# Performance work log

Hardware: AMD Instinct MI355X
Metric: run time of the kernel (lower is better)

The kernel has to match this reference:

```python
import jax, jax.numpy as jnp
import numpy as np

B, N, H = 2, 160, 256
F = 512  # num_hidden_fc
C3 = 3 * H  # concatenated modality feature
C6 = 2 * C3  # pairwise feature


def setup_inputs() -> dict:
    key = jax.random.key(0)
    ks = jax.random.split(key, 16)
    s1 = 1.0 / np.sqrt(C6)
    s2 = 1.0 / np.sqrt(F)
    inp = {
        "geometry": jax.random.normal(ks[0], (B, N, H), jnp.float32),
        "appearance": jax.random.normal(ks[1], (B, N, H), jnp.float32),
        "content": jax.random.normal(ks[2], (B, N, H), jnp.float32),
    }
    for i, name in enumerate(["cell", "row", "col"]):
        inp[f"{name}_W1"] = jax.random.normal(ks[3 + 4 * i], (C6, F), jnp.float32) * s1
        inp[f"{name}_b1"] = jnp.zeros((F,), jnp.float32)
        inp[f"{name}_W2"] = jax.random.normal(ks[4 + 4 * i], (F, 2), jnp.float32) * s2
        inp[f"{name}_b2"] = jnp.zeros((2,), jnp.float32)
    return inp


def _head(x, W1, b1, W2, b2):
    h = jax.nn.relu(jnp.einsum("bpc,cf->bpf", x, W1) + b1)
    return jax.nn.softmax(jnp.einsum("bpf,fk->bpk", h, W2) + b2, axis=-1)


def reference(geometry, appearance, content,
              cell_W1, cell_b1, cell_W2, cell_b2,
              row_W1, row_b1, row_W2, row_b2,
              col_W1, col_b1, col_W2, col_b2):
    emb = jnp.concatenate([geometry, appearance, content], axis=-1)  # (B,N,3H)
    b, n, c = emb.shape
    # pairs[b,i,j] = concat(emb[b,j], emb[b,i])  (matches unsqueeze(1)/unsqueeze(2) order)
    e_j = jnp.broadcast_to(emb[:, None, :, :], (b, n, n, c))
    e_i = jnp.broadcast_to(emb[:, :, None, :], (b, n, n, c))
    emb_pairs = jnp.concatenate([e_j, e_i], axis=-1).reshape(b, n * n, 2 * c)
    cell_logits = _head(emb_pairs, cell_W1, cell_b1, cell_W2, cell_b2)
    row_logits = _head(emb_pairs, row_W1, row_b1, row_W2, row_b2)
    col_logits = _head(emb_pairs, col_W1, col_b1, col_W2, col_b2)
    return cell_logits, row_logits, col_logits, emb_pairs
```

## Files before the change

### kernel.cpp

```cpp
#include <hip/hip_runtime.h>

#define NB 2
#define NN 160
#define NPAIR (NN*NN)
#define OUT_PAIRS_OFF 307200

__global__ __launch_bounds__(256) void proj_fp32_kernel(
    const float* __restrict__ geo, const float* __restrict__ app,
    const float* __restrict__ con,
    const float* __restrict__ w1c, const float* __restrict__ w1r,
    const float* __restrict__ w1l,
    const float* __restrict__ b1c, const float* __restrict__ b1r,
    const float* __restrict__ b1l,
    float* __restrict__ proj)
{
    __shared__ float As[64][17];
    __shared__ float Bs[16][68];

    const int tid = threadIdx.x;
    const int m0 = blockIdx.x * 64;
    const int n0 = blockIdx.y * 64;
    const int t  = n0 >> 10;
    const int s  = (n0 >> 9) & 1;
    const int f0 = n0 & 511;

    const float* w1 = (t == 0) ? w1c : ((t == 1) ? w1r : w1l);
    const float* b1 = (t == 0) ? b1c : ((t == 1) ? b1r : b1l);

    const int ty = tid >> 4, tx = tid & 15;
    const int ar = tid >> 2, ac = (tid & 3) * 4;
    const int bk = tid >> 4, bn = (tid & 15) * 4;

    float acc[4][4] = {};

    for (int k0 = 0; k0 < 768; k0 += 16) {
        {
            const int c = k0 + ac;
            const int m = c >> 8, off = c & 255;
            const float* src = ((m == 0) ? geo : (m == 1) ? app : con)
                               + (size_t)(m0 + ar) * 256 + off;
            const float4 v = *(const float4*)src;
            As[ar][ac + 0] = v.x; As[ar][ac + 1] = v.y;
            As[ar][ac + 2] = v.z; As[ar][ac + 3] = v.w;
        }
        {
            const float4 v = *(const float4*)(
                w1 + (size_t)(s * 768 + k0 + bk) * 512 + f0 + bn);
            Bs[bk][bn + 0] = v.x; Bs[bk][bn + 1] = v.y;
            Bs[bk][bn + 2] = v.z; Bs[bk][bn + 3] = v.w;
        }
        __syncthreads();

        #pragma unroll
        for (int k = 0; k < 16; ++k) {
            const float4 b = *(const float4*)&Bs[k][tx * 4];
            const float a0 = As[ty * 4 + 0][k];
            const float a1 = As[ty * 4 + 1][k];
            const float a2 = As[ty * 4 + 2][k];
            const float a3 = As[ty * 4 + 3][k];
            acc[0][0] += a0 * b.x; acc[0][1] += a0 * b.y;
            acc[0][2] += a0 * b.z; acc[0][3] += a0 * b.w;
            acc[1][0] += a1 * b.x; acc[1][1] += a1 * b.y;
            acc[1][2] += a1 * b.z; acc[1][3] += a1 * b.w;
            acc[2][0] += a2 * b.x; acc[2][1] += a2 * b.y;
            acc[2][2] += a2 * b.z; acc[2][3] += a2 * b.w;
            acc[3][0] += a3 * b.x; acc[3][1] += a3 * b.y;
            acc[3][2] += a3 * b.z; acc[3][3] += a3 * b.w;
        }
        __syncthreads();
    }

    float4 bias = {0.f, 0.f, 0.f, 0.f};
    if (s == 0) bias = *(const float4*)&b1[f0 + tx * 4];

    #pragma unroll
    for (int r = 0; r < 4; ++r) {
        float4 o;
        o.x = acc[r][0] + bias.x; o.y = acc[r][1] + bias.y;
        o.z = acc[r][2] + bias.z; o.w = acc[r][3] + bias.w;
        *(float4*)&proj[(size_t)((t * 2 + s) * 320 + m0 + ty * 4 + r) * 512
                        + f0 + tx * 4] = o;
    }
}

__global__ __launch_bounds__(64) void heads_kernel(
    const float* __restrict__ proj,
    const float* __restrict__ w2c, const float* __restrict__ b2c,
    const float* __restrict__ w2r, const float* __restrict__ b2r,
    const float* __restrict__ w2l, const float* __restrict__ b2l,
    float* __restrict__ out)
{
    __shared__ float P1s[8][516];
    __shared__ float P2s[8][516];
    __shared__ float w2s[1024];
    __shared__ float b2s[2];

    const int tid = threadIdx.x;
    const int bid = blockIdx.x;
    const int b   = bid / 400;
    const int rem = bid - b * 400;
    const int it  = rem / 20;
    const int jt  = rem - it * 20;
    const int i0 = it * 8, j0 = jt * 8;
    const int ii = tid >> 3, jj = tid & 7;

    #pragma unroll
    for (int t = 0; t < 3; ++t) {
        const float* w2 = (t == 0) ? w2c : ((t == 1) ? w2r : w2l);
        const float* b2 = (t == 0) ? b2c : ((t == 1) ? b2r : b2l);

        for (int u = tid; u < 2048; u += 64) {
            const int tile = u >> 10;
            const int r    = (u >> 7) & 7;
            const int f4   = u & 127;
            const int p    = b * 160 + (tile ? (i0 + r) : (j0 + r));
            const float4 v = *(const float4*)(
                proj + ((size_t)((t * 2 + tile) * 320 + p)) * 512 + f4 * 4);
            float* dst = tile ? &P2s[r][f4 * 4] : &P1s[r][f4 * 4];
            *(float4*)dst = v;
        }
        for (int u = tid; u < 256; u += 64)
            *(float4*)&w2s[u * 4] = *(const float4*)(w2 + u * 4);
        if (tid < 2) b2s[tid] = b2[tid];
        __syncthreads();

        float a0 = b2s[0], a1 = b2s[1];
        for (int f = 0; f < 512; f += 4) {
            const float4 p1 = *(const float4*)&P1s[jj][f];
            const float4 p2 = *(const float4*)&P2s[ii][f];
            const float4 wA = *(const float4*)&w2s[f * 2];
            const float4 wB = *(const float4*)&w2s[f * 2 + 4];
            const float h0 = fmaxf(p1.x + p2.x, 0.f);
            const float h1 = fmaxf(p1.y + p2.y, 0.f);
            const float h2 = fmaxf(p1.z + p2.z, 0.f);
            const float h3 = fmaxf(p1.w + p2.w, 0.f);
            a0 += h0 * wA.x + h1 * wA.z + h2 * wB.x + h3 * wB.z;
            a1 += h0 * wA.y + h1 * wA.w + h2 * wB.y + h3 * wB.w;
        }

        const float mx = fmaxf(a0, a1);
        const float e0 = __expf(a0 - mx);
        const float e1 = __expf(a1 - mx);
        const float rs = 1.f / (e0 + e1);

        const int pr = b * 25600 + (i0 + ii) * 160 + (j0 + jj);
        float2 o; o.x = e0 * rs; o.y = e1 * rs;
        ((float2*)out)[t * 51200 + pr] = o;
        __syncthreads();
    }
}

__global__ __launch_bounds__(256) void pairs_kernel(
    const float* __restrict__ geo, const float* __restrict__ app,
    const float* __restrict__ con,
    float4* __restrict__ outp)
{
    const int idx = blockIdx.x * 256 + threadIdx.x;
    const int row = idx / 384;
    const int c   = idx - row * 384;
    const int b   = row / 25600;
    const int rem = row - b * 25600;
    const int i   = rem / 160;
    const int j   = rem - i * 160;

    int cc = c, pt = j;
    if (c >= 192) { pt = i; cc = c - 192; }
    const int m   = cc >> 6;
    const int off = cc & 63;
    const float* src = ((m == 0) ? geo : (m == 1) ? app : con)
                       + ((size_t)(b * 160 + pt)) * 256 + off * 4;

    outp[idx] = *(const float4*)src;
}

extern "C" void kernel_launch(void* const* d_in, const int* in_sizes, int n_in,
                              void* d_out, int out_size, void* d_ws, size_t ws_size,
                              hipStream_t stream)
{
    const float* geo = (const float*)d_in[0];
    const float* app = (const float*)d_in[1];
    const float* con = (const float*)d_in[2];
    const float* w1c = (const float*)d_in[3];
    const float* b1c = (const float*)d_in[4];
    const float* w2c = (const float*)d_in[5];
    const float* b2c = (const float*)d_in[6];
    const float* w1r = (const float*)d_in[7];
    const float* b1r = (const float*)d_in[8];
    const float* w2r = (const float*)d_in[9];
    const float* b2r = (const float*)d_in[10];
    const float* w1l = (const float*)d_in[11];
    const float* b1l = (const float*)d_in[12];
    const float* w2l = (const float*)d_in[13];
    const float* b2l = (const float*)d_in[14];

    float* out = (float*)d_out;

    float* proj = out + OUT_PAIRS_OFF;

    proj_fp32_kernel<<<dim3(5, 48), 256, 0, stream>>>(
        geo, app, con, w1c, w1r, w1l, b1c, b1r, b1l, proj);

    heads_kernel<<<800, 64, 0, stream>>>(
        proj, w2c, b2c, w2r, b2r, w2l, b2l, out);

    pairs_kernel<<<76800, 256, 0, stream>>>(
        geo, app, con, (float4*)(out + OUT_PAIRS_OFF));
}
```

Before: 446.0 us.

## Use bf16 MFMA for projection, fuse pair writes into heads, sigmoid-difference softmax

The fp32 tiled projection GEMM is replaced with a one-wave bf16 MFMA kernel (16x16x32) that converts inputs and weights to bf16 in registers. The pair-broadcast output copy is merged into the heads kernel, so each of the 800 blocks writes its own 64 rows of emb_pairs, and proj moves to workspace memory. The 2-way softmax now reduces to a single logit difference, with one dot product and a sigmoid. Together these remove one launch and roughly halve the head arithmetic, at the cost of bf16 rounding in the projection and much less parallelism for the 157 MB pair write, which now uses only 800 blocks of 64 threads.

```diff
diff --git a/kernel.cpp b/kernel.cpp
--- a/kernel.cpp
+++ b/kernel.cpp
@@ -5,7 +5,17 @@
 #define NPAIR (NN*NN)
 #define OUT_PAIRS_OFF 307200
 
-__global__ __launch_bounds__(256) void proj_fp32_kernel(
+typedef __attribute__((ext_vector_type(8))) short bf16x8;
+typedef __attribute__((ext_vector_type(4))) float f32x4;
+
+static __device__ __forceinline__ ushort f2bf(float x) {
+    union { float f; uint u; } c; c.f = x;
+    uint u = c.u;
+    u += 0x7fffu + ((u >> 16) & 1u);
+    return (ushort)(u >> 16);
+}
+
+__global__ __launch_bounds__(64) void proj_mfma_kernel(
     const float* __restrict__ geo, const float* __restrict__ app,
     const float* __restrict__ con,
     const float* __restrict__ w1c, const float* __restrict__ w1r,
@@ -14,76 +24,69 @@
     const float* __restrict__ b1l,
     float* __restrict__ proj)
 {
-    __shared__ float As[64][17];
-    __shared__ float Bs[16][68];
-
-    const int tid = threadIdx.x;
-    const int m0 = blockIdx.x * 64;
-    const int n0 = blockIdx.y * 64;
-    const int t  = n0 >> 10;
-    const int s  = (n0 >> 9) & 1;
+    const int lane = threadIdx.x;
+    const int m0 = blockIdx.x * 32;
+    const int n0 = blockIdx.y * 16;
+    const int t = n0 >> 10;
+    const int s = (n0 >> 9) & 1;
     const int f0 = n0 & 511;
 
     const float* w1 = (t == 0) ? w1c : ((t == 1) ? w1r : w1l);
     const float* b1 = (t == 0) ? b1c : ((t == 1) ? b1r : b1l);
 
-    const int ty = tid >> 4, tx = tid & 15;
-    const int ar = tid >> 2, ac = (tid & 3) * 4;
-    const int bk = tid >> 4, bn = (tid & 15) * 4;
+    const int col = lane & 15;
+    const int quad = lane >> 4;
 
-    float acc[4][4] = {};
+    f32x4 acc0 = {0.f, 0.f, 0.f, 0.f};
+    f32x4 acc1 = {0.f, 0.f, 0.f, 0.f};
 
-    for (int k0 = 0; k0 < 768; k0 += 16) {
-        {
-            const int c = k0 + ac;
-            const int m = c >> 8, off = c & 255;
-            const float* src = ((m == 0) ? geo : (m == 1) ? app : con)
-                               + (size_t)(m0 + ar) * 256 + off;
-            const float4 v = *(const float4*)src;
-            As[ar][ac + 0] = v.x; As[ar][ac + 1] = v.y;
-            As[ar][ac + 2] = v.z; As[ar][ac + 3] = v.w;
-        }
-        {
-            const float4 v = *(const float4*)(
-                w1 + (size_t)(s * 768 + k0 + bk) * 512 + f0 + bn);
-            Bs[bk][bn + 0] = v.x; Bs[bk][bn + 1] = v.y;
-            Bs[bk][bn + 2] = v.z; Bs[bk][bn + 3] = v.w;
-        }
-        __syncthreads();
+    const float* wbase = w1 + (size_t)(s * 768) * 512 + f0 + col;
+    const int p0 = m0 + col;
+    const int p1 = p0 + 16;
 
+    for (int k0 = 0; k0 < 768; k0 += 32) {
+        const int klane = k0 + quad * 8;
+        const int mod = klane >> 8;
+        const int off = klane & 255;
+        const float* src = (mod == 0) ? geo : ((mod == 1) ? app : con);
+
+        const float4 a0lo = *(const float4*)(src + (size_t)p0 * 256 + off);
+        const float4 a0hi = *(const float4*)(src + (size_t)p0 * 256 + off + 4);
+        const float4 a1lo = *(const float4*)(src + (size_t)p1 * 256 + off);
+        const float4 a1hi = *(const float4*)(src + (size_t)p1 * 256 + off + 4);
+
+        bf16x8 af0, af1, bfrag;
+        af0[0] = (short)f2bf(a0lo.x); af0[1] = (short)f2bf(a0lo.y);
+        af0[2] = (short)f2bf(a0lo.z); af0[3] = (short)f2bf(a0lo.w);
+        af0[4] = (short)f2bf(a0hi.x); af0[5] = (short)f2bf(a0hi.y);
+        af0[6] = (short)f2bf(a0hi.z); af0[7] = (short)f2bf(a0hi.w);
+        af1[0] = (short)f2bf(a1lo.x); af1[1] = (short)f2bf(a1lo.y);
+        af1[2] = (short)f2bf(a1lo.z); af1[3] = (short)f2bf(a1lo.w);
+        af1[4] = (short)f2bf(a1hi.x); af1[5] = (short)f2bf(a1hi.y);
+        af1[6] = (short)f2bf(a1hi.z); af1[7] = (short)f2bf(a1hi.w);
+
+        const float* wp = wbase + (size_t)klane * 512;
         #pragma unroll
-        for (int k = 0; k < 16; ++k) {
-            const float4 b = *(const float4*)&Bs[k][tx * 4];
-            const float a0 = As[ty * 4 + 0][k];
-            const float a1 = As[ty * 4 + 1][k];
-            const float a2 = As[ty * 4 + 2][k];
-            const float a3 = As[ty * 4 + 3][k];
-            acc[0][0] += a0 * b.x; acc[0][1] += a0 * b.y;
-            acc[0][2] += a0 * b.z; acc[0][3] += a0 * b.w;
-            acc[1][0] += a1 * b.x; acc[1][1] += a1 * b.y;
-            acc[1][2] += a1 * b.z; acc[1][3] += a1 * b.w;
-            acc[2][0] += a2 * b.x; acc[2][1] += a2 * b.y;
-            acc[2][2] += a2 * b.z; acc[2][3] += a2 * b.w;
-            acc[3][0] += a3 * b.x; acc[3][1] += a3 * b.y;
-            acc[3][2] += a3 * b.z; acc[3][3] += a3 * b.w;
-        }
-        __syncthreads();
+        for (int j = 0; j < 8; ++j) bfrag[j] = (short)f2bf(wp[(size_t)j * 512]);
+
+        acc0 = __builtin_amdgcn_mfma_f32_16x16x32_bf16(af0, bfrag, acc0, 0, 0, 0);
+        acc1 = __builtin_amdgcn_mfma_f32_16x16x32_bf16(af1, bfrag, acc1, 0, 0, 0);
     }
 
-    float4 bias = {0.f, 0.f, 0.f, 0.f};
-    if (s == 0) bias = *(const float4*)&b1[f0 + tx * 4];
+    float bias = 0.f;
+    if (s == 0) bias = b1[f0 + col];
 
+    const size_t base = (size_t)(t * 2 + s) * 320 * 512 + f0 + col;
     #pragma unroll
     for (int r = 0; r < 4; ++r) {
-        float4 o;
-        o.x = acc[r][0] + bias.x; o.y = acc[r][1] + bias.y;
-        o.z = acc[r][2] + bias.z; o.w = acc[r][3] + bias.w;
-        *(float4*)&proj[(size_t)((t * 2 + s) * 320 + m0 + ty * 4 + r) * 512
-                        + f0 + tx * 4] = o;
+        proj[base + (size_t)(m0 + quad * 4 + r) * 512]      = acc0[r] + bias;
+        proj[base + (size_t)(m0 + 16 + quad * 4 + r) * 512] = acc1[r] + bias;
     }
 }
 
-__global__ __launch_bounds__(64) void heads_kernel(
+__global__ __launch_bounds__(64) void fused_kernel(
+    const float* __restrict__ geo, const float* __restrict__ app,
+    const float* __restrict__ con,
     const float* __restrict__ proj,
     const float* __restrict__ w2c, const float* __restrict__ b2c,
     const float* __restrict__ w2r, const float* __restrict__ b2r,
@@ -92,8 +95,7 @@
 {
     __shared__ float P1s[8][516];
     __shared__ float P2s[8][516];
-    __shared__ float w2s[1024];
-    __shared__ float b2s[2];
+    __shared__ float wds[512];
 
     const int tid = threadIdx.x;
     const int bid = blockIdx.x;
@@ -103,6 +105,24 @@
     const int jt  = rem - it * 20;
     const int i0 = it * 8, j0 = jt * 8;
     const int ii = tid >> 3, jj = tid & 7;
+
+    float4* pout = (float4*)(out + OUT_PAIRS_OFF);
+    for (int r8 = 0; r8 < 8; ++r8) {
+        #pragma unroll
+        for (int jl = 0; jl < 8; ++jl) {
+            const int row = b * 25600 + (i0 + r8) * 160 + (j0 + jl);
+            for (int u = tid; u < 384; u += 64) {
+                const int half = (u >= 192) ? 1 : 0;
+                const int cc   = u - half * 192;
+                const int m    = cc >> 6;
+                const int off  = cc & 63;
+                const int pt   = half ? (i0 + r8) : (j0 + jl);
+                const float* src = ((m == 0) ? geo : (m == 1) ? app : con)
+                                   + ((size_t)(b * 160 + pt)) * 256 + off * 4;
+                pout[(size_t)row * 384 + u] = *(const float4*)src;
+            }
+        }
+    }
 
     #pragma unroll
     for (int t = 0; t < 3; ++t) {
@@ -119,58 +139,33 @@
             float* dst = tile ? &P2s[r][f4 * 4] : &P1s[r][f4 * 4];
             *(float4*)dst = v;
         }
-        for (int u = tid; u < 256; u += 64)
-            *(float4*)&w2s[u * 4] = *(const float4*)(w2 + u * 4);
-        if (tid < 2) b2s[tid] = b2[tid];
+        for (int u = tid; u < 512; u += 64)
+            wds[u] = w2[u * 2 + 1] - w2[u * 2];
         __syncthreads();
 
-        float a0 = b2s[0], a1 = b2s[1];
+        float d = b2[1] - b2[0];
         for (int f = 0; f < 512; f += 4) {
             const float4 p1 = *(const float4*)&P1s[jj][f];
             const float4 p2 = *(const float4*)&P2s[ii][f];
-            const float4 wA = *(const float4*)&w2s[f * 2];
-            const float4 wB = *(const float4*)&w2s[f * 2 + 4];
-            const float h0 = fmaxf(p1.x + p2.x, 0.f);
-            const float h1 = fmaxf(p1.y + p2.y, 0.f);
-            const float h2 = fmaxf(p1.z + p2.z, 0.f);
-            const float h3 = fmaxf(p1.w + p2.w, 0.f);
-            a0 += h0 * wA.x + h1 * wA.z + h2 * wB.x + h3 * wB.z;
-            a1 += h0 * wA.y + h1 * wA.w + h2 * wB.y + h3 * wB.w;
+            const float4 wd = *(const float4*)&wds[f];
+            d += fmaxf(p1.x + p2.x, 0.f) * wd.x;
+            d += fmaxf(p1.y + p2.y, 0.f) * wd.y;
+            d += fmaxf(p1.z + p2.z, 0.f) * wd.z;
+            d += fmaxf(p1.w + p2.w, 0.f) * wd.w;
         }
 
-        const float mx = fmaxf(a0, a1);
-        const float e0 = __expf(a0 - mx);
-        const float e1 = __expf(a1 - mx);
-        const float rs = 1.f / (e0 + e1);
+        const float e   = __expf(-fabsf(d));
+        const float inv = 1.f / (1.f + e);
+        const float phi = inv;
+        const float plo = e * inv;
+        float2 o;
+        o.x = (d >= 0.f) ? plo : phi;
+        o.y = (d >= 0.f) ? phi : plo;
 
         const int pr = b * 25600 + (i0 + ii) * 160 + (j0 + jj);
-        float2 o; o.x = e0 * rs; o.y = e1 * rs;
         ((float2*)out)[t * 51200 + pr] = o;
         __syncthreads();
     }
-}
-
-__global__ __launch_bounds__(256) void pairs_kernel(
-    const float* __restrict__ geo, const float* __restrict__ app,
-    const float* __restrict__ con,
-    float4* __restrict__ outp)
-{
-    const int idx = blockIdx.x * 256 + threadIdx.x;
-    const int row = idx / 384;
-    const int c   = idx - row * 384;
-    const int b   = row / 25600;
-    const int rem = row - b * 25600;
-    const int i   = rem / 160;
-    const int j   = rem - i * 160;
-
-    int cc = c, pt = j;
-    if (c >= 192) { pt = i; cc = c - 192; }
-    const int m   = cc >> 6;
-    const int off = cc & 63;
-    const float* src = ((m == 0) ? geo : (m == 1) ? app : con)
-                       + ((size_t)(b * 160 + pt)) * 256 + off * 4;
-
-    outp[idx] = *(const float4*)src;
 }
 
 extern "C" void kernel_launch(void* const* d_in, const int* in_sizes, int n_in,
@@ -193,16 +188,12 @@
     const float* w2l = (const float*)d_in[13];
     const float* b2l = (const float*)d_in[14];
 
-    float* out = (float*)d_out;
+    float* out  = (float*)d_out;
+    float* proj = (float*)d_ws;
 
-    float* proj = out + OUT_PAIRS_OFF;
-
-    proj_fp32_kernel<<<dim3(5, 48), 256, 0, stream>>>(
+    proj_mfma_kernel<<<dim3(10, 192), 64, 0, stream>>>(
         geo, app, con, w1c, w1r, w1l, b1c, b1r, b1l, proj);
 
-    heads_kernel<<<800, 64, 0, stream>>>(
-        proj, w2c, b2c, w2r, b2r, w2l, b2l, out);
-
-    pairs_kernel<<<76800, 256, 0, stream>>>(
-        geo, app, con, (float4*)(out + OUT_PAIRS_OFF));
+    fused_kernel<<<800, 64, 0, stream>>>(
+        geo, app, con, proj, w2c, b2c, w2r, b2r, w2l, b2l, out);
 }
```

Result: slower. 466.1 us (+4.5%).
